# Kernel optimization log

Measured on AMD Instinct MI355X. Metric: run time of the kernel, lower is better.

## Reference

```python
import jax, jax.numpy as jnp
import numpy as np

F_DIM = 64; HID = 64; HEADS = 2; DH = 32; NG = 4; EPS = 1e-5; SCALE = 8.0  # sqrt(hid_dim)
B = 4; H = 64; W = 64; S = 8; CIN = 64


def _ln(x, g, b):
    mu = x.mean(-1, keepdims=True)
    var = ((x - mu) ** 2).mean(-1, keepdims=True)
    return (x - mu) * jax.lax.rsqrt(var + EPS) * g + b


def _gn(x, g, b):
    # x: [b, C, H, W]; normalize per group over (C/NG, H, W)
    bb, c, hh, ww = x.shape
    xg = x.reshape(bb, NG, -1)
    mu = xg.mean(-1, keepdims=True)
    var = ((xg - mu) ** 2).mean(-1, keepdims=True)
    xn = ((xg - mu) * jax.lax.rsqrt(var + EPS)).reshape(bb, c, hh, ww)
    return xn * g[None, :, None, None] + b[None, :, None, None]


def _mha(xq, xkv, qw, qb, kw, kb, vw, vb, ow, ob):
    # per-head attention with scaling by sqrt(hid_dim) (as in the source)
    q = xq @ qw + qb
    k = xkv @ kw + kb
    v = xkv @ vw + vb
    bb, l, _ = q.shape
    m = k.shape[1]
    qh = q.reshape(bb, l, HEADS, DH)
    kh = k.reshape(bb, m, HEADS, DH)
    vh = v.reshape(bb, m, HEADS, DH)
    s = jnp.einsum('blhd,bmhd->bhlm', qh, kh) / SCALE
    p = jax.nn.softmax(s, axis=-1)
    z = jnp.einsum('bhlm,bmhd->blhd', p, vh).reshape(bb, l, HID)
    return z @ ow + ob


def setup_inputs() -> dict:
    key = jax.random.key(0)
    ks = jax.random.split(key, 34)
    p = lambda k, shp: (jax.random.normal(k, shp, jnp.float32) * 0.02)
    d = {
        'x': jax.random.normal(ks[0], (B, H, W, F_DIM), jnp.float32),
        'slots': jax.random.normal(ks[1], (B, S, CIN), jnp.float32),
        'conv1_w': p(ks[2], (F_DIM, F_DIM)), 'conv1_b': p(ks[3], (F_DIM,)),
        'conv2_w': p(ks[4], (F_DIM, F_DIM)), 'conv2_b': p(ks[5], (F_DIM,)),
        'gn_g': jnp.ones((F_DIM,), jnp.float32), 'gn_b': jnp.zeros((F_DIM,), jnp.float32),
        'ln2_g': jnp.ones((F_DIM,), jnp.float32), 'ln2_b': jnp.zeros((F_DIM,), jnp.float32),
        'ln3_g': jnp.ones((F_DIM,), jnp.float32), 'ln3_b': jnp.zeros((F_DIM,), jnp.float32),
        'ln4_g': jnp.ones((F_DIM,), jnp.float32), 'ln4_b': jnp.zeros((F_DIM,), jnp.float32),
        'sa_qw': p(ks[6], (F_DIM, HID)), 'sa_qb': p(ks[7], (HID,)),
        'sa_kw': p(ks[8], (F_DIM, HID)), 'sa_kb': p(ks[9], (HID,)),
        'sa_vw': p(ks[10], (F_DIM, HID)), 'sa_vb': p(ks[11], (HID,)),
        'sa_ow': p(ks[12], (HID, F_DIM)), 'sa_ob': p(ks[13], (F_DIM,)),
        'ca_qw': p(ks[14], (F_DIM, HID)), 'ca_qb': p(ks[15], (HID,)),
        'ca_kw': p(ks[16], (CIN, HID)), 'ca_kb': p(ks[17], (HID,)),
        'ca_vw': p(ks[18], (CIN, HID)), 'ca_vb': p(ks[19], (HID,)),
        'ca_ow': p(ks[20], (HID, F_DIM)), 'ca_ob': p(ks[21], (F_DIM,)),
        'ff1_w': p(ks[22], (F_DIM, F_DIM)), 'ff1_b': p(ks[23], (F_DIM,)),
    }
    return d


def reference(x, slots, conv1_w, conv1_b, conv2_w, conv2_b, gn_g, gn_b,
              ln2_g, ln2_b, ln3_g, ln3_b, ln4_g, ln4_b,
              sa_qw, sa_qb, sa_kw, sa_kb, sa_vw, sa_vb, sa_ow, sa_ob,
              ca_qw, ca_qb, ca_kw, ca_kb, ca_vw, ca_vb, ca_ow, ca_ob,
              ff1_w, ff1_b):
    b, h, w, f = x.shape
    xc = jnp.transpose(x, (0, 3, 1, 2))               # [b,f,h,w]
    xc = _gn(xc, gn_g, gn_b)
    xc = jnp.einsum('bchw,oc->bohw', xc, conv1_w) + conv1_b[None, :, None, None]
    # faithful to torch: .contiguous().view(b,-1,f) on channels-first layout
    xs = xc.reshape(b, h * w, f)
    # repeat = 1
    xs = jax.nn.gelu(_ln(_mha(xs, xs, sa_qw, sa_qb, sa_kw, sa_kb, sa_vw, sa_vb, sa_ow, sa_ob), ln2_g, ln2_b) + xs, approximate=False)
    xs = _ln(_mha(xs, slots, ca_qw, ca_qb, ca_kw, ca_kb, ca_vw, ca_vb, ca_ow, ca_ob), ln3_g, ln3_b) + xs
    xs = _ln(xs @ ff1_w + ff1_b, ln4_g, ln4_b) + xs
    xo = jnp.transpose(xs.reshape(b, h, w, f), (0, 3, 1, 2))
    xo = jnp.einsum('bchw,oc->bohw', xo, conv2_w) + conv2_b[None, :, None, None]
    return jnp.transpose(xo, (0, 2, 3, 1))
```

## Files before the change

### kernel.cpp

```cpp
#include <hip/hip_runtime.h>
#include <hip/hip_bf16.h>
#include <math.h>

#define NBATCH 4
#define LTOK   4096
#define FD     64
#define KSPLIT 8
#define NIT    8

typedef __attribute__((ext_vector_type(8))) short short8v;
typedef __attribute__((ext_vector_type(4))) float f32x4;
typedef __attribute__((ext_vector_type(16))) float f32x16;

static __device__ inline uint32_t packbf2(float a, float b) {
    float2 f; f.x = a; f.y = b;
    __hip_bfloat162 h = __float22bfloat162_rn(f);
    uint32_t u; __builtin_memcpy(&u, &h, 4);
    return u;
}
static __device__ inline ushort packbf1(float a) {
    __hip_bfloat16 h = __float2bfloat16(a);
    ushort u; __builtin_memcpy(&u, &h, 2);
    return u;
}
static __device__ inline float gelu_exact(float y) {
    return 0.5f * y * (1.0f + erff(y * 0.70710678118654752f));
}

__global__ void gn_part_kernel(const float* __restrict__ x,
                               float* __restrict__ partS, float* __restrict__ partSS) {
    const int b = blockIdx.x >> 6, c = blockIdx.x & 63;
    const int t = threadIdx.x, l = t & 63, wv = t >> 6;
    const float4* xb = (const float4*)(x + (size_t)b * 262144) + (size_t)c * 1024;
    float s = 0.f, ss = 0.f;
#pragma unroll
    for (int k = 0; k < 4; k++) {
        float4 v = xb[t + 256 * k];
        s += (v.x + v.y) + (v.z + v.w);
        ss += (v.x * v.x + v.y * v.y) + (v.z * v.z + v.w * v.w);
    }
#pragma unroll
    for (int o = 0; o < 4; o++) {
        const int off = (int[]){1, 2, 16, 32}[o];
        s += __shfl_xor(s, off, 64);
        ss += __shfl_xor(ss, off, 64);
    }
    __shared__ float ls_s[4][4], ls_ss[4][4];
    if ((l & 51) == 0) { ls_s[wv][(l >> 2) & 3] = s; ls_ss[wv][(l >> 2) & 3] = ss; }
    __syncthreads();
    if (t < 4) {
        float S = 0.f, SS = 0.f;
#pragma unroll
        for (int w2 = 0; w2 < 4; w2++) { S += ls_s[w2][t]; SS += ls_ss[w2][t]; }
        partS[b * 256 + t * 64 + c] = S;
        partSS[b * 256 + t * 64 + c] = SS;
    }
}

__global__ void gn_conv1_kernel(const float* __restrict__ x,
                                const float* __restrict__ partS, const float* __restrict__ partSS,
                                const float* __restrict__ gg, const float* __restrict__ gb,
                                const float* __restrict__ w, const float* __restrict__ bias,
                                float* __restrict__ out) {
    const int b = blockIdx.x >> 6, i = blockIdx.x & 63;
    const int t = threadIdx.x;
    __shared__ float xn[64][65];
    __shared__ float wsm[64][64];
    __shared__ float sm[4], sr[4];
    {
        float sv = partS[b * 256 + t];
        float ssv = partSS[b * 256 + t];
        for (int o = 32; o; o >>= 1) { sv += __shfl_xor(sv, o, 64); ssv += __shfl_xor(ssv, o, 64); }
        if ((t & 63) == 0) {
            float mean = sv * (1.f / 65536.f);
            float var = ssv * (1.f / 65536.f) - mean * mean;
            sm[t >> 6] = mean;
            sr[t >> 6] = rsqrtf(var + 1e-5f);
        }
    }
    __syncthreads();
    {
        const int j = t >> 2, c0 = (t & 3) * 16, g = c0 >> 4;
        const float mean = sm[g], rstd = sr[g];
        const float* src = x + (((size_t)b * 64 + i) * 64 + j) * 64 + c0;
#pragma unroll
        for (int k = 0; k < 4; k++) {
            float4 v = *(const float4*)(src + 4 * k);
            xn[j][c0 + 4 * k + 0] = (v.x - mean) * rstd * gg[c0 + 4 * k + 0] + gb[c0 + 4 * k + 0];
            xn[j][c0 + 4 * k + 1] = (v.y - mean) * rstd * gg[c0 + 4 * k + 1] + gb[c0 + 4 * k + 1];
            xn[j][c0 + 4 * k + 2] = (v.z - mean) * rstd * gg[c0 + 4 * k + 2] + gb[c0 + 4 * k + 2];
            xn[j][c0 + 4 * k + 3] = (v.w - mean) * rstd * gg[c0 + 4 * k + 3] + gb[c0 + 4 * k + 3];
        }
        const int o = t >> 2, cc0 = (t & 3) * 16;
#pragma unroll
        for (int k = 0; k < 16; k++) wsm[cc0 + k][o] = w[o * 64 + cc0 + k];
    }
    __syncthreads();
    const int jj = t & 63, olo = (t >> 6) * 16;
    float acc[16];
#pragma unroll
    for (int oi = 0; oi < 16; oi++) acc[oi] = bias[olo + oi];
    for (int c = 0; c < 64; c++) {
        float xv = xn[jj][c];
#pragma unroll
        for (int oi = 0; oi < 16; oi++) acc[oi] += xv * wsm[c][olo + oi];
    }
#pragma unroll
    for (int oi = 0; oi < 16; oi++)
        out[((size_t)b * LTOK + (size_t)(olo + oi) * 64 + i) * 64 + jj] = acc[oi];
}

__global__ void qkv_kernel(const float* __restrict__ in,
                           const float* __restrict__ qw, const float* __restrict__ qb,
                           const float* __restrict__ kw, const float* __restrict__ kb,
                           const float* __restrict__ vw, const float* __restrict__ vb,
                           ushort* __restrict__ Qo, ushort* __restrict__ Ko, ushort* __restrict__ VTg) {
    __shared__ float xt[64][68];
    __shared__ float wt[64][64];
    __shared__ ushort vtr[64 * 72];
    const int t = threadIdx.x;
    const int ph = blockIdx.y;
    const size_t tok0 = (size_t)blockIdx.x * 64;
    const int b = blockIdx.x >> 6;
    const int tokb0 = (blockIdx.x & 63) * 64;
    const int r = t >> 2, cq = t & 3, olo = cq * 16;
    const float* W = (ph == 0) ? qw : (ph == 1) ? kw : vw;
    const float* Bb = (ph == 0) ? qb : (ph == 1) ? kb : vb;
    {
        const float4* src = (const float4*)(in + tok0 * 64) + (size_t)t * 4;
        float4* dst = (float4*)&xt[r][olo];
#pragma unroll
        for (int k = 0; k < 4; k++) dst[k] = src[k];
        const float4* ws2 = (const float4*)W + (size_t)t * 4;
        float4* wd = (float4*)wt + (size_t)t * 4;
#pragma unroll
        for (int k = 0; k < 4; k++) wd[k] = ws2[k];
    }
    __syncthreads();
    float acc[16];
#pragma unroll
    for (int k = 0; k < 4; k++) {
        float4 bv = *(const float4*)(Bb + olo + 4 * k);
        acc[4 * k] = bv.x; acc[4 * k + 1] = bv.y; acc[4 * k + 2] = bv.z; acc[4 * k + 3] = bv.w;
    }
    for (int f = 0; f < 64; f++) {
        float xv = xt[r][f];
#pragma unroll
        for (int oi = 0; oi < 16; oi++) acc[oi] += xv * wt[f][olo + oi];
    }
    if (ph < 2) {
        const float sc = (ph == 0) ? 0.180336880111f : 1.0f;
        uint32_t u[8];
#pragma unroll
        for (int i = 0; i < 8; i++) u[i] = packbf2(acc[2 * i] * sc, acc[2 * i + 1] * sc);
        ushort* op = (ph == 0 ? Qo : Ko) + (tok0 + r) * 64 + olo;
        *(uint4*)op = make_uint4(u[0], u[1], u[2], u[3]);
        *(uint4*)(op + 8) = make_uint4(u[4], u[5], u[6], u[7]);
    } else {
#pragma unroll
        for (int oi = 0; oi < 16; oi++) vtr[(olo + oi) * 72 + r] = packbf1(acc[oi]);
        __syncthreads();
        const int o = t >> 2, ch = t & 3;
        uint4 a0 = *(const uint4*)&vtr[o * 72 + ch * 16];
        uint4 a1 = *(const uint4*)&vtr[o * 72 + ch * 16 + 8];
        ushort* op = VTg + (size_t)(b * 64 + o) * 4096 + tokb0 + ch * 16;
        *(uint4*)op = a0;
        *(uint4*)(op + 8) = a1;
    }
}

__global__ __launch_bounds__(256) void flash_mfma(const ushort* __restrict__ Q,
                                                  const ushort* __restrict__ K,
                                                  const ushort* __restrict__ VTg,
                                                  ushort* __restrict__ ZpAll,
                                                  float* __restrict__ Ls) {
    const int qt = blockIdx.x;
    const int bh = blockIdx.y;
    const int ks = blockIdx.z;
    const int b = bh >> 1, h = bh & 1;
    const int t = threadIdx.x;
    const int w = t >> 6, l = t & 63, lq = l & 31, sig = l >> 5;

    __shared__ ushort KsB[2][2048];
    __shared__ ushort VTB[2][2048];

    const size_t base = (size_t)b * LTOK * 64 + h * 32;
    const size_t vrow0 = (size_t)(b * 64 + h * 32);

    const int qrow = qt * 128 + w * 32 + lq;
    const short8v qf0 = *(const short8v*)(Q + base + (size_t)qrow * 64 + 8 * sig);
    const short8v qf1 = *(const short8v*)(Q + base + (size_t)qrow * 64 + 16 + 8 * sig);

    const int krow = t >> 2, kdg = t & 3;
    const int koff = ((krow << 5) + kdg * 8) ^ ((krow & 7) << 3);
    const int vrow = t >> 3, vc8 = t & 7;
    const int voff = ((vrow << 6) + vc8 * 8) ^ ((vrow & 7) << 3);
    const ushort* kgp = K + base + (size_t)(ks * NIT * 64 + krow) * 64 + kdg * 8;
    const ushort* vgp = VTg + (vrow0 + vrow) * 4096 + ks * NIT * 64 + vc8 * 8;

    *(uint4*)&KsB[0][koff] = *(const uint4*)kgp;  kgp += 64 * 64;
    *(uint4*)&VTB[0][voff] = *(const uint4*)vgp;  vgp += 64;

    f32x16 accZ;
#pragma unroll
    for (int i = 0; i < 16; i++) accZ[i] = 0.f;
    f32x16 zero16;
#pragma unroll
    for (int i = 0; i < 16; i++) zero16[i] = 0.f;
    float lacc = 0.0f;

    auto body = [&](const ushort* Kc, const ushort* Vc, ushort* Kn, ushort* Vn, bool pref) {
        __syncthreads();
        uint4 kq = make_uint4(0, 0, 0, 0), vq = make_uint4(0, 0, 0, 0);
        if (pref) {
            kq = *(const uint4*)kgp; kgp += 64 * 64;
            vq = *(const uint4*)vgp; vgp += 64;
        }
#pragma unroll
        for (int kb2 = 0; kb2 < 2; kb2++) {
            const int kb = kb2 * 32;
            const int kr = kb + lq;
            const short8v aK0 = *(const short8v*)&Kc[((kr << 5) + 8 * sig) ^ ((kr & 7) << 3)];
            const short8v aK1 = *(const short8v*)&Kc[((kr << 5) + 16 + 8 * sig) ^ ((kr & 7) << 3)];
            f32x16 st = __builtin_amdgcn_mfma_f32_32x32x16_bf16(aK0, qf0, zero16, 0, 0, 0);
            st = __builtin_amdgcn_mfma_f32_32x32x16_bf16(aK1, qf1, st, 0, 0, 0);
            uint32_t pk[8];
#pragma unroll
            for (int i = 0; i < 8; i++) {
                float p0 = __builtin_amdgcn_exp2f(st[2 * i]);
                float p1 = __builtin_amdgcn_exp2f(st[2 * i + 1]);
                lacc += p0 + p1;
                pk[i] = packbf2(p0, p1);
            }
            uint32_t a0w0 = pk[0], a0w2 = pk[2];
            uint32_t a0w1 = pk[1], a0w3 = pk[3];
            uint32_t a1w0 = pk[4], a1w2 = pk[6];
            uint32_t a1w1 = pk[5], a1w3 = pk[7];
            asm volatile("v_permlane32_swap_b32 %0, %1" : "+v"(a0w0), "+v"(a0w2));
            asm volatile("v_permlane32_swap_b32 %0, %1" : "+v"(a0w1), "+v"(a0w3));
            asm volatile("v_permlane32_swap_b32 %0, %1" : "+v"(a1w0), "+v"(a1w2));
            asm volatile("v_permlane32_swap_b32 %0, %1" : "+v"(a1w1), "+v"(a1w3));
            uint4 A0 = make_uint4(a0w0, a0w1, a0w2, a0w3);
            uint4 A1 = make_uint4(a1w0, a1w1, a1w2, a1w3);
            short8v aP0, aP1;
            __builtin_memcpy(&aP0, &A0, 16);
            __builtin_memcpy(&aP1, &A1, 16);
            const short8v vt0 = *(const short8v*)&Vc[((lq << 6) + kb + 8 * sig) ^ ((lq & 7) << 3)];
            const short8v vt1 = *(const short8v*)&Vc[((lq << 6) + kb + 16 + 8 * sig) ^ ((lq & 7) << 3)];
            accZ = __builtin_amdgcn_mfma_f32_32x32x16_bf16(aP0, vt0, accZ, 0, 0, 0);
            accZ = __builtin_amdgcn_mfma_f32_32x32x16_bf16(aP1, vt1, accZ, 0, 0, 0);
        }
        if (pref) {
            *(uint4*)&Kn[koff] = kq;
            *(uint4*)&Vn[voff] = vq;
        }
    };

#pragma unroll 1
    for (int it = 0; it < NIT / 2; it++) {
        body(KsB[0], VTB[0], KsB[1], VTB[1], true);
        body(KsB[1], VTB[1], KsB[0], VTB[0], it < NIT / 2 - 1);
    }

    ushort* Zo = ZpAll + (size_t)ks * (NBATCH * LTOK * FD);
#pragma unroll
    for (int r = 0; r < 16; r++) {
        const int qr = qt * 128 + w * 32 + (r & 3) + 8 * (r >> 2) + 4 * sig;
        Zo[base + (size_t)qr * 64 + lq] = packbf1(accZ[r]);
    }
    lacc += __shfl_xor(lacc, 32, 64);
    if (l < 32)
        Ls[ks * 32768 + bh * 4096 + qt * 128 + w * 32 + lq] = lacc;
}

__global__ __launch_bounds__(256) void tail_fused(
    const ushort* __restrict__ ZpAll,
    const float* __restrict__ Ls, const float* __restrict__ xs0,
    const float* __restrict__ slots,
    const float* __restrict__ ckw, const float* __restrict__ ckb,
    const float* __restrict__ cvw, const float* __restrict__ cvb,
    const float* __restrict__ ow, const float* __restrict__ ob,
    const float* __restrict__ g2, const float* __restrict__ b2,
    const float* __restrict__ qw, const float* __restrict__ qb,
    const float* __restrict__ cow, const float* __restrict__ cob,
    const float* __restrict__ g3, const float* __restrict__ b3,
    const float* __restrict__ fw, const float* __restrict__ fb,
    const float* __restrict__ g4, const float* __restrict__ b4,
    const float* __restrict__ cw, const float* __restrict__ cb,
    float* __restrict__ out)
{
    const int t = threadIdx.x;
    const size_t tok0 = (size_t)blockIdx.x * 32;
    const int b = blockIdx.x >> 7;
    const int r = t >> 3, c = t & 7, olo = c * 8;
    __shared__ float xt[32][68];
    __shared__ float wt[64][64];
    __shared__ float kcs[512], vcs[512], sls[512];

    float acc[8], res[8];

    auto stage_w = [&](const float* W) {
#pragma unroll
        for (int k = 0; k < 4; k++)
            ((float4*)wt)[4 * t + k] = ((const float4*)W)[4 * t + k];
    };
    auto stage_x_res = [&]() {
        float4* xd = (float4*)&xt[r][olo];
        xd[0] = make_float4(res[0], res[1], res[2], res[3]);
        xd[1] = make_float4(res[4], res[5], res[6], res[7]);
    };
    auto load8 = [&](float* dst, const float* p) {
        float4 u0 = *(const float4*)(p + olo);
        float4 u1 = *(const float4*)(p + olo + 4);
        dst[0] = u0.x; dst[1] = u0.y; dst[2] = u0.z; dst[3] = u0.w;
        dst[4] = u1.x; dst[5] = u1.y; dst[6] = u1.z; dst[7] = u1.w;
    };
    auto mm = [&](const float* bias) {
        load8(acc, bias);
        for (int f = 0; f < 64; f++) {
            float xv = xt[r][f];
#pragma unroll
            for (int oi = 0; oi < 8; oi++) acc[oi] += xv * wt[f][olo + oi];
        }
    };
    auto ln = [&](const float* gv, const float* bv, bool dogelu) {
        float s1 = 0.f, s2 = 0.f;
#pragma unroll
        for (int oi = 0; oi < 8; oi++) { s1 += acc[oi]; s2 += acc[oi] * acc[oi]; }
#pragma unroll
        for (int o = 1; o <= 4; o <<= 1) {
            s1 += __shfl_xor(s1, o, 64);
            s2 += __shfl_xor(s2, o, 64);
        }
        float mean = s1 * (1.f / 64.f);
        float var = s2 * (1.f / 64.f) - mean * mean;
        float rstd = rsqrtf(var + 1e-5f);
        float gl[8], bl[8];
        load8(gl, gv); load8(bl, bv);
#pragma unroll
        for (int oi = 0; oi < 8; oi++) {
            float y = (acc[oi] - mean) * rstd * gl[oi] + bl[oi] + res[oi];
            res[oi] = dogelu ? gelu_exact(y) : y;
        }
    };

    {
        if (t < 128) ((float4*)sls)[t] = ((const float4*)(slots + (size_t)b * 512))[t];
        float zs[8];
#pragma unroll
        for (int j = 0; j < 8; j++) zs[j] = 0.f;
#pragma unroll
        for (int kb = 0; kb < KSPLIT; kb++) {
            const uint4 u = *(const uint4*)(ZpAll + (size_t)kb * (NBATCH * LTOK * FD)
                                            + tok0 * 64 + (size_t)t * 8);
            const uint32_t arr[4] = {u.x, u.y, u.z, u.w};
#pragma unroll
            for (int j = 0; j < 4; j++) {
                zs[2 * j]     += __uint_as_float(arr[j] << 16);
                zs[2 * j + 1] += __uint_as_float(arr[j] & 0xffff0000u);
            }
        }
        const int hh = olo >> 5;
        const int bh_ = b * 2 + hh;
        const int tokb = (blockIdx.x & 127) * 32 + r;
        float lt = 0.f;
#pragma unroll
        for (int kb = 0; kb < KSPLIT; kb++) lt += Ls[kb * 32768 + bh_ * 4096 + tokb];
        const float inv = 1.0f / lt;
        float4* xd = (float4*)&xt[r][olo];
        xd[0] = make_float4(zs[0] * inv, zs[1] * inv, zs[2] * inv, zs[3] * inv);
        xd[1] = make_float4(zs[4] * inv, zs[5] * inv, zs[6] * inv, zs[7] * inv);
        stage_w(ow);
        float4 r0 = *(const float4*)(xs0 + (tok0 + r) * 64 + olo);
        float4 r1 = *(const float4*)(xs0 + (tok0 + r) * 64 + olo + 4);
        res[0] = r0.x; res[1] = r0.y; res[2] = r0.z; res[3] = r0.w;
        res[4] = r1.x; res[5] = r1.y; res[6] = r1.z; res[7] = r1.w;
    }
    __syncthreads();
    for (int jo = t; jo < 512; jo += 256) {
        const int j = jo >> 6, o = jo & 63;
        float ak = ckb[o], av = cvb[o];
#pragma unroll 8
        for (int c2 = 0; c2 < 64; c2++) {
            float sv = sls[j * 64 + c2];
            ak += sv * ckw[c2 * 64 + o];
            av += sv * cvw[c2 * 64 + o];
        }
        kcs[jo] = ak; vcs[jo] = av;
    }
    mm(ob);
    ln(g2, b2, true);

    __syncthreads();
    stage_x_res();
    stage_w(qw);
    __syncthreads();
    mm(qb);
    {
        float p[8];
        float mx = -3.0e38f;
#pragma unroll
        for (int j = 0; j < 8; j++) {
            float d = 0.f;
#pragma unroll
            for (int i2 = 0; i2 < 8; i2++) d += acc[i2] * kcs[j * 64 + olo + i2];
            d += __shfl_xor(d, 1, 64);
            d += __shfl_xor(d, 2, 64);
            d *= 0.125f;
            p[j] = d;
            mx = fmaxf(mx, d);
        }
        float es = 0.f;
#pragma unroll
        for (int j = 0; j < 8; j++) { p[j] = __expf(p[j] - mx); es += p[j]; }
        float inv = 1.f / es;
#pragma unroll
        for (int oi = 0; oi < 8; oi++) {
            float z = 0.f;
#pragma unroll
            for (int j = 0; j < 8; j++) z += p[j] * vcs[j * 64 + olo + oi];
            acc[oi] = z * inv;
        }
    }

    __syncthreads();
    {
        float4* xd = (float4*)&xt[r][olo];
        xd[0] = make_float4(acc[0], acc[1], acc[2], acc[3]);
        xd[1] = make_float4(acc[4], acc[5], acc[6], acc[7]);
    }
    stage_w(cow);
    __syncthreads();
    mm(cob);
    ln(g3, b3, false);

    __syncthreads();
    stage_x_res();
    stage_w(fw);
    __syncthreads();
    mm(fb);
    ln(g4, b4, false);

    __syncthreads();
    stage_x_res();
    {
        const int o5 = t >> 2, c5 = (t & 3) * 16;
#pragma unroll
        for (int k = 0; k < 16; k++) wt[c5 + k][o5] = cw[o5 * 64 + c5 + k];
    }
    __syncthreads();
    mm(cb);
    float* op = out + (tok0 + r) * 64 + olo;
    *(float4*)op = make_float4(acc[0], acc[1], acc[2], acc[3]);
    *(float4*)(op + 4) = make_float4(acc[4], acc[5], acc[6], acc[7]);
}

extern "C" void kernel_launch(void* const* d_in, const int* in_sizes, int n_in,
                              void* d_out, int out_size, void* d_ws, size_t ws_size,
                              hipStream_t stream) {
    const float* x       = (const float*)d_in[0];
    const float* slots   = (const float*)d_in[1];
    const float* conv1_w = (const float*)d_in[2];
    const float* conv1_b = (const float*)d_in[3];
    const float* conv2_w = (const float*)d_in[4];
    const float* conv2_b = (const float*)d_in[5];
    const float* gn_g    = (const float*)d_in[6];
    const float* gn_b    = (const float*)d_in[7];
    const float* ln2_g   = (const float*)d_in[8];
    const float* ln2_b   = (const float*)d_in[9];
    const float* ln3_g   = (const float*)d_in[10];
    const float* ln3_b   = (const float*)d_in[11];
    const float* ln4_g   = (const float*)d_in[12];
    const float* ln4_b   = (const float*)d_in[13];
    const float* sa_qw   = (const float*)d_in[14];
    const float* sa_qb   = (const float*)d_in[15];
    const float* sa_kw   = (const float*)d_in[16];
    const float* sa_kb   = (const float*)d_in[17];
    const float* sa_vw   = (const float*)d_in[18];
    const float* sa_vb   = (const float*)d_in[19];
    const float* sa_ow   = (const float*)d_in[20];
    const float* sa_ob   = (const float*)d_in[21];
    const float* ca_qw   = (const float*)d_in[22];
    const float* ca_qb   = (const float*)d_in[23];
    const float* ca_kw   = (const float*)d_in[24];
    const float* ca_kb   = (const float*)d_in[25];
    const float* ca_vw   = (const float*)d_in[26];
    const float* ca_vb   = (const float*)d_in[27];
    const float* ca_ow   = (const float*)d_in[28];
    const float* ca_ob   = (const float*)d_in[29];
    const float* ff1_w   = (const float*)d_in[30];
    const float* ff1_b   = (const float*)d_in[31];

    float* ws = (float*)d_ws;
    const size_t NBUF = (size_t)NBATCH * LTOK * FD;
    float* partS  = ws;
    float* partSS = ws + 1024;
    float* A      = ws + 4096;
    ushort* Kb    = (ushort*)(A + NBUF);
    ushort* VTgb  = Kb + NBUF;
    ushort* Qb    = VTgb + NBUF;
    ushort* ZpAll = Qb + NBUF;
    float* Ls     = (float*)(ZpAll + (size_t)KSPLIT * NBUF);

    gn_part_kernel<<<256, 256, 0, stream>>>(x, partS, partSS);
    gn_conv1_kernel<<<256, 256, 0, stream>>>(x, partS, partSS, gn_g, gn_b, conv1_w, conv1_b, A);
    qkv_kernel<<<dim3(256, 3), 256, 0, stream>>>(A, sa_qw, sa_qb, sa_kw, sa_kb, sa_vw, sa_vb, Qb, Kb, VTgb);
    flash_mfma<<<dim3(32, 8, KSPLIT), 256, 0, stream>>>(Qb, Kb, VTgb, ZpAll, Ls);
    tail_fused<<<512, 256, 0, stream>>>(ZpAll, Ls, A, slots,
                                        ca_kw, ca_kb, ca_vw, ca_vb,
                                        sa_ow, sa_ob, ln2_g, ln2_b,
                                        ca_qw, ca_qb, ca_ow, ca_ob, ln3_g, ln3_b,
                                        ff1_w, ff1_b, ln4_g, ln4_b,
                                        conv2_w, conv2_b, (float*)d_out);
}
```

Baseline: 90.85 us.

## Store K/V in MFMA fragment layout and drop LDS staging in flash kernel

The QKV kernel now writes K and V directly in a per-lane MFMA fragment order, so the attention kernel can load operands straight from global memory into registers. This removes the shared-memory double buffer and its barriers. Each wave now handles two 32-row query tiles that share the same K/V fragments, halving the block count and doubling reuse per load, with launch bounds raised to four blocks per CU. The risks are more register pressure and no explicit prefetch of global loads, so latency is left to occupancy and the unrolled loop.

```diff
diff --git a/kernel.cpp b/kernel.cpp
--- a/kernel.cpp
+++ b/kernel.cpp
@@ -6,7 +6,7 @@
 #define LTOK   4096
 #define FD     64
 #define KSPLIT 8
-#define NIT    8
+#define MBLK   16
 
 typedef __attribute__((ext_vector_type(8))) short short8v;
 typedef __attribute__((ext_vector_type(4))) float f32x4;
@@ -114,7 +114,7 @@
                            const float* __restrict__ qw, const float* __restrict__ qb,
                            const float* __restrict__ kw, const float* __restrict__ kb,
                            const float* __restrict__ vw, const float* __restrict__ vb,
-                           ushort* __restrict__ Qo, ushort* __restrict__ Ko, ushort* __restrict__ VTg) {
+                           ushort* __restrict__ Qo, ushort* __restrict__ KF, ushort* __restrict__ VF) {
     __shared__ float xt[64][68];
     __shared__ float wt[64][64];
     __shared__ ushort vtr[64 * 72];
@@ -148,32 +148,45 @@
 #pragma unroll
         for (int oi = 0; oi < 16; oi++) acc[oi] += xv * wt[f][olo + oi];
     }
-    if (ph < 2) {
-        const float sc = (ph == 0) ? 0.180336880111f : 1.0f;
+    if (ph == 0) {
+        const float sc = 0.180336880111f;
         uint32_t u[8];
 #pragma unroll
         for (int i = 0; i < 8; i++) u[i] = packbf2(acc[2 * i] * sc, acc[2 * i + 1] * sc);
-        ushort* op = (ph == 0 ? Qo : Ko) + (tok0 + r) * 64 + olo;
+        ushort* op = Qo + (tok0 + r) * 64 + olo;
         *(uint4*)op = make_uint4(u[0], u[1], u[2], u[3]);
         *(uint4*)(op + 8) = make_uint4(u[4], u[5], u[6], u[7]);
+    } else if (ph == 1) {
+        uint32_t u[8];
+#pragma unroll
+        for (int i = 0; i < 8; i++) u[i] = packbf2(acc[2 * i], acc[2 * i + 1]);
+        const int tokb = tokb0 + r;
+        const int m = tokb >> 5, tq = tokb & 31;
+        const int hh = cq >> 1, f = cq & 1;
+        const int bhh = b * 2 + hh;
+        ushort* p0 = KF + ((size_t)(bhh * 128 + m) * 2 + f) * 512;
+        *(uint4*)(p0 + tq * 8)        = make_uint4(u[0], u[1], u[2], u[3]);
+        *(uint4*)(p0 + (32 + tq) * 8) = make_uint4(u[4], u[5], u[6], u[7]);
     } else {
 #pragma unroll
         for (int oi = 0; oi < 16; oi++) vtr[(olo + oi) * 72 + r] = packbf1(acc[oi]);
         __syncthreads();
         const int o = t >> 2, ch = t & 3;
+        const int lq2 = o & 31, hh = o >> 5, bhh = b * 2 + hh;
+        const int m = (tokb0 >> 5) + (ch >> 1), f = ch & 1;
         uint4 a0 = *(const uint4*)&vtr[o * 72 + ch * 16];
         uint4 a1 = *(const uint4*)&vtr[o * 72 + ch * 16 + 8];
-        ushort* op = VTg + (size_t)(b * 64 + o) * 4096 + tokb0 + ch * 16;
-        *(uint4*)op = a0;
-        *(uint4*)(op + 8) = a1;
-    }
-}
-
-__global__ __launch_bounds__(256) void flash_mfma(const ushort* __restrict__ Q,
-                                                  const ushort* __restrict__ K,
-                                                  const ushort* __restrict__ VTg,
-                                                  ushort* __restrict__ ZpAll,
-                                                  float* __restrict__ Ls) {
+        ushort* p0 = VF + ((size_t)(bhh * 128 + m) * 2 + f) * 512;
+        *(uint4*)(p0 + lq2 * 8)        = a0;
+        *(uint4*)(p0 + (32 + lq2) * 8) = a1;
+    }
+}
+
+__global__ __launch_bounds__(256, 4) void flash_mfma(const ushort* __restrict__ Q,
+                                                     const ushort* __restrict__ KF,
+                                                     const ushort* __restrict__ VF,
+                                                     ushort* __restrict__ ZpAll,
+                                                     float* __restrict__ Ls) {
     const int qt = blockIdx.x;
     const int bh = blockIdx.y;
     const int ks = blockIdx.z;
@@ -181,96 +194,80 @@
     const int t = threadIdx.x;
     const int w = t >> 6, l = t & 63, lq = l & 31, sig = l >> 5;
 
-    __shared__ ushort KsB[2][2048];
-    __shared__ ushort VTB[2][2048];
-
     const size_t base = (size_t)b * LTOK * 64 + h * 32;
-    const size_t vrow0 = (size_t)(b * 64 + h * 32);
-
-    const int qrow = qt * 128 + w * 32 + lq;
-    const short8v qf0 = *(const short8v*)(Q + base + (size_t)qrow * 64 + 8 * sig);
-    const short8v qf1 = *(const short8v*)(Q + base + (size_t)qrow * 64 + 16 + 8 * sig);
-
-    const int krow = t >> 2, kdg = t & 3;
-    const int koff = ((krow << 5) + kdg * 8) ^ ((krow & 7) << 3);
-    const int vrow = t >> 3, vc8 = t & 7;
-    const int voff = ((vrow << 6) + vc8 * 8) ^ ((vrow & 7) << 3);
-    const ushort* kgp = K + base + (size_t)(ks * NIT * 64 + krow) * 64 + kdg * 8;
-    const ushort* vgp = VTg + (vrow0 + vrow) * 4096 + ks * NIT * 64 + vc8 * 8;
-
-    *(uint4*)&KsB[0][koff] = *(const uint4*)kgp;  kgp += 64 * 64;
-    *(uint4*)&VTB[0][voff] = *(const uint4*)vgp;  vgp += 64;
-
-    f32x16 accZ;
-#pragma unroll
-    for (int i = 0; i < 16; i++) accZ[i] = 0.f;
-    f32x16 zero16;
-#pragma unroll
-    for (int i = 0; i < 16; i++) zero16[i] = 0.f;
-    float lacc = 0.0f;
-
-    auto body = [&](const ushort* Kc, const ushort* Vc, ushort* Kn, ushort* Vn, bool pref) {
-        __syncthreads();
-        uint4 kq = make_uint4(0, 0, 0, 0), vq = make_uint4(0, 0, 0, 0);
-        if (pref) {
-            kq = *(const uint4*)kgp; kgp += 64 * 64;
-            vq = *(const uint4*)vgp; vgp += 64;
-        }
-#pragma unroll
-        for (int kb2 = 0; kb2 < 2; kb2++) {
-            const int kb = kb2 * 32;
-            const int kr = kb + lq;
-            const short8v aK0 = *(const short8v*)&Kc[((kr << 5) + 8 * sig) ^ ((kr & 7) << 3)];
-            const short8v aK1 = *(const short8v*)&Kc[((kr << 5) + 16 + 8 * sig) ^ ((kr & 7) << 3)];
-            f32x16 st = __builtin_amdgcn_mfma_f32_32x32x16_bf16(aK0, qf0, zero16, 0, 0, 0);
-            st = __builtin_amdgcn_mfma_f32_32x32x16_bf16(aK1, qf1, st, 0, 0, 0);
-            uint32_t pk[8];
-#pragma unroll
-            for (int i = 0; i < 8; i++) {
-                float p0 = __builtin_amdgcn_exp2f(st[2 * i]);
-                float p1 = __builtin_amdgcn_exp2f(st[2 * i + 1]);
-                lacc += p0 + p1;
-                pk[i] = packbf2(p0, p1);
-            }
-            uint32_t a0w0 = pk[0], a0w2 = pk[2];
-            uint32_t a0w1 = pk[1], a0w3 = pk[3];
-            uint32_t a1w0 = pk[4], a1w2 = pk[6];
-            uint32_t a1w1 = pk[5], a1w3 = pk[7];
-            asm volatile("v_permlane32_swap_b32 %0, %1" : "+v"(a0w0), "+v"(a0w2));
-            asm volatile("v_permlane32_swap_b32 %0, %1" : "+v"(a0w1), "+v"(a0w3));
-            asm volatile("v_permlane32_swap_b32 %0, %1" : "+v"(a1w0), "+v"(a1w2));
-            asm volatile("v_permlane32_swap_b32 %0, %1" : "+v"(a1w1), "+v"(a1w3));
-            uint4 A0 = make_uint4(a0w0, a0w1, a0w2, a0w3);
-            uint4 A1 = make_uint4(a1w0, a1w1, a1w2, a1w3);
-            short8v aP0, aP1;
-            __builtin_memcpy(&aP0, &A0, 16);
-            __builtin_memcpy(&aP1, &A1, 16);
-            const short8v vt0 = *(const short8v*)&Vc[((lq << 6) + kb + 8 * sig) ^ ((lq & 7) << 3)];
-            const short8v vt1 = *(const short8v*)&Vc[((lq << 6) + kb + 16 + 8 * sig) ^ ((lq & 7) << 3)];
-            accZ = __builtin_amdgcn_mfma_f32_32x32x16_bf16(aP0, vt0, accZ, 0, 0, 0);
-            accZ = __builtin_amdgcn_mfma_f32_32x32x16_bf16(aP1, vt1, accZ, 0, 0, 0);
-        }
-        if (pref) {
-            *(uint4*)&Kn[koff] = kq;
-            *(uint4*)&Vn[voff] = vq;
-        }
+    const int q0 = qt * 256 + w * 64;
+
+    const ushort* qp = Q + base + (size_t)(q0 + lq) * 64 + 8 * sig;
+    const short8v qfA0 = *(const short8v*)(qp);
+    const short8v qfA1 = *(const short8v*)(qp + 16);
+    const short8v qfB0 = *(const short8v*)(qp + 32 * 64);
+    const short8v qfB1 = *(const short8v*)(qp + 32 * 64 + 16);
+
+    const ushort* kfp = KF + ((size_t)(bh * 128 + ks * MBLK) * 2) * 512 + l * 8;
+    const ushort* vfp = VF + ((size_t)(bh * 128 + ks * MBLK) * 2) * 512 + l * 8;
+
+    f32x16 accA, accB, zero16;
+#pragma unroll
+    for (int i = 0; i < 16; i++) { accA[i] = 0.f; accB[i] = 0.f; zero16[i] = 0.f; }
+    float laccA = 0.f, laccB = 0.f;
+
+    auto mk_aP = [&](const f32x16& st, float& lacc, short8v& aP0v, short8v& aP1v) {
+        uint32_t pk[8];
+#pragma unroll
+        for (int i = 0; i < 8; i++) {
+            float p0 = __builtin_amdgcn_exp2f(st[2 * i]);
+            float p1 = __builtin_amdgcn_exp2f(st[2 * i + 1]);
+            lacc += p0 + p1;
+            pk[i] = packbf2(p0, p1);
+        }
+        uint32_t w0 = pk[0], w2 = pk[2], w1 = pk[1], w3 = pk[3];
+        uint32_t x0 = pk[4], x2 = pk[6], x1 = pk[5], x3 = pk[7];
+        asm volatile("v_permlane32_swap_b32 %0, %1" : "+v"(w0), "+v"(w2));
+        asm volatile("v_permlane32_swap_b32 %0, %1" : "+v"(w1), "+v"(w3));
+        asm volatile("v_permlane32_swap_b32 %0, %1" : "+v"(x0), "+v"(x2));
+        asm volatile("v_permlane32_swap_b32 %0, %1" : "+v"(x1), "+v"(x3));
+        uint4 A0 = make_uint4(w0, w1, w2, w3), A1 = make_uint4(x0, x1, x2, x3);
+        __builtin_memcpy(&aP0v, &A0, 16);
+        __builtin_memcpy(&aP1v, &A1, 16);
     };
 
-#pragma unroll 1
-    for (int it = 0; it < NIT / 2; it++) {
-        body(KsB[0], VTB[0], KsB[1], VTB[1], true);
-        body(KsB[1], VTB[1], KsB[0], VTB[0], it < NIT / 2 - 1);
+#pragma unroll 4
+    for (int m = 0; m < MBLK; m++) {
+        const short8v kf0 = *(const short8v*)kfp;
+        const short8v kf1 = *(const short8v*)(kfp + 512);
+        const short8v vf0 = *(const short8v*)vfp;
+        const short8v vf1 = *(const short8v*)(vfp + 512);
+        kfp += 1024; vfp += 1024;
+
+        f32x16 st = __builtin_amdgcn_mfma_f32_32x32x16_bf16(kf0, qfA0, zero16, 0, 0, 0);
+        st = __builtin_amdgcn_mfma_f32_32x32x16_bf16(kf1, qfA1, st, 0, 0, 0);
+        short8v aPA0, aPA1;
+        mk_aP(st, laccA, aPA0, aPA1);
+
+        f32x16 st2 = __builtin_amdgcn_mfma_f32_32x32x16_bf16(kf0, qfB0, zero16, 0, 0, 0);
+        st2 = __builtin_amdgcn_mfma_f32_32x32x16_bf16(kf1, qfB1, st2, 0, 0, 0);
+        short8v aPB0, aPB1;
+        mk_aP(st2, laccB, aPB0, aPB1);
+
+        accA = __builtin_amdgcn_mfma_f32_32x32x16_bf16(aPA0, vf0, accA, 0, 0, 0);
+        accA = __builtin_amdgcn_mfma_f32_32x32x16_bf16(aPA1, vf1, accA, 0, 0, 0);
+        accB = __builtin_amdgcn_mfma_f32_32x32x16_bf16(aPB0, vf0, accB, 0, 0, 0);
+        accB = __builtin_amdgcn_mfma_f32_32x32x16_bf16(aPB1, vf1, accB, 0, 0, 0);
     }
 
     ushort* Zo = ZpAll + (size_t)ks * (NBATCH * LTOK * FD);
 #pragma unroll
     for (int r = 0; r < 16; r++) {
-        const int qr = qt * 128 + w * 32 + (r & 3) + 8 * (r >> 2) + 4 * sig;
-        Zo[base + (size_t)qr * 64 + lq] = packbf1(accZ[r]);
-    }
-    lacc += __shfl_xor(lacc, 32, 64);
-    if (l < 32)
-        Ls[ks * 32768 + bh * 4096 + qt * 128 + w * 32 + lq] = lacc;
+        const int qr = q0 + (r & 3) + 8 * (r >> 2) + 4 * sig;
+        Zo[base + (size_t)qr * 64 + lq] = packbf1(accA[r]);
+        Zo[base + (size_t)(qr + 32) * 64 + lq] = packbf1(accB[r]);
+    }
+    laccA += __shfl_xor(laccA, 32, 64);
+    laccB += __shfl_xor(laccB, 32, 64);
+    if (l < 32) {
+        Ls[ks * 32768 + bh * 4096 + q0 + lq] = laccA;
+        Ls[ks * 32768 + bh * 4096 + q0 + 32 + lq] = laccB;
+    }
 }
 
 __global__ __launch_bounds__(256) void tail_fused(
@@ -496,16 +493,16 @@
     float* partS  = ws;
     float* partSS = ws + 1024;
     float* A      = ws + 4096;
-    ushort* Kb    = (ushort*)(A + NBUF);
-    ushort* VTgb  = Kb + NBUF;
-    ushort* Qb    = VTgb + NBUF;
+    ushort* KF    = (ushort*)(A + NBUF);
+    ushort* VF    = KF + NBUF;
+    ushort* Qb    = VF + NBUF;
     ushort* ZpAll = Qb + NBUF;
     float* Ls     = (float*)(ZpAll + (size_t)KSPLIT * NBUF);
 
     gn_part_kernel<<<256, 256, 0, stream>>>(x, partS, partSS);
     gn_conv1_kernel<<<256, 256, 0, stream>>>(x, partS, partSS, gn_g, gn_b, conv1_w, conv1_b, A);
-    qkv_kernel<<<dim3(256, 3), 256, 0, stream>>>(A, sa_qw, sa_qb, sa_kw, sa_kb, sa_vw, sa_vb, Qb, Kb, VTgb);
-    flash_mfma<<<dim3(32, 8, KSPLIT), 256, 0, stream>>>(Qb, Kb, VTgb, ZpAll, Ls);
+    qkv_kernel<<<dim3(256, 3), 256, 0, stream>>>(A, sa_qw, sa_qb, sa_kw, sa_kb, sa_vw, sa_vb, Qb, KF, VF);
+    flash_mfma<<<dim3(16, 8, KSPLIT), 256, 0, stream>>>(Qb, KF, VF, ZpAll, Ls);
     tail_fused<<<512, 256, 0, stream>>>(ZpAll, Ls, A, slots,
                                         ca_kw, ca_kb, ca_vw, ca_vb,
                                         sa_ow, sa_ob, ln2_g, ln2_b,
```

Result: faster. 88.25 us (-2.9%).
